# Kernel tuning notes

Hardware: AMD Instinct MI355X
Metric: run time of the kernel (lower is better)

## Reference

```python
import jax, jax.numpy as jnp
import numpy as np

T = 128          # target_size
START = 126      # tag_map['start_token']
STOP = 127       # tag_map['stop_token'] == 'end_token'
NEG = -10000.0


def setup_inputs() -> dict:
    key = jax.random.key(0)
    k1, k2, k3 = jax.random.split(key, 3)
    B, S = 256, 512
    feats = jax.random.normal(k1, (B, S, T), dtype=jnp.float32)
    transitions = jax.random.normal(k2, (T, T), dtype=jnp.float32)
    # constraints from __init__: nothing transitions into start, nothing leaves end
    transitions = transitions.at[START, :].set(NEG)
    transitions = transitions.at[:, STOP].set(NEG)
    targets = jax.random.randint(k3, (B, S), 0, 126, dtype=jnp.int32)
    return {"feats": feats, "transitions": transitions, "targets": targets}


def _crf_nll(feats, transitions, targets):
    B, S, _ = feats.shape
    # ---- forward algorithm (log partition) ----
    init = jnp.full((B, T), NEG, dtype=feats.dtype).at[:, START].set(0.0)

    def step(fv, f_t):  # fv [B,T], f_t [B,T]
        # new[b, tag] = logsumexp_prev(fv[b, prev] + trans[tag, prev]) + f_t[b, tag]
        new = jax.nn.logsumexp(fv[:, None, :] + transitions[None, :, :], axis=2) + f_t
        return new, None

    fv, _ = jax.lax.scan(step, init, jnp.swapaxes(feats, 0, 1))  # scan over S
    alpha = jax.nn.logsumexp(fv + transitions[STOP][None, :], axis=1)  # [B]

    # ---- gold path score ----
    start_col = jnp.full((B, 1), START, dtype=targets.dtype)
    tags_ext = jnp.concatenate([start_col, targets], axis=1)  # [B, S+1]
    trans_score = transitions[tags_ext[:, 1:], tags_ext[:, :-1]].sum(axis=1)  # [B]
    emit_score = jnp.take_along_axis(feats, targets[..., None].astype(jnp.int32), axis=2)[..., 0].sum(axis=1)
    gold = trans_score + emit_score + transitions[STOP, tags_ext[:, -1]]  # [B]

    # module returns gold_score - alpha
    return gold - alpha


def reference(feats, transitions, targets):
    return _crf_nll(feats, transitions, targets)
```

## Files before the change

### kernel.cpp

```cpp
#include <hip/hip_runtime.h>
#include <math.h>

#define TT 128
#define SS 512
#define NB 256
#define START_TAG 126
#define STOP_TAG 127
#define NEGV -10000.0f

__device__ __forceinline__ float rlane(float v, int lane) {
    return __int_as_float(__builtin_amdgcn_readlane(__float_as_int(v), lane));
}
__device__ __forceinline__ float wave_max(float v) {
#pragma unroll
    for (int off = 32; off >= 1; off >>= 1) v = fmaxf(v, __shfl_xor(v, off));
    return v;
}
__device__ __forceinline__ float wave_sum(float v) {
#pragma unroll
    for (int off = 32; off >= 1; off >>= 1) v += __shfl_xor(v, off);
    return v;
}

__global__ __launch_bounds__(512, 2) void crf_fwd_kernel(
    const float* __restrict__ feats,
    const float* __restrict__ trans,
    const int*   __restrict__ targets,
    float*       __restrict__ out)
{
    const int t = threadIdx.x;
    const int b = blockIdx.x;
    const int w = t >> 6;
    const int l = t & 63;
    const int group = w >> 2;
    const int g = w & 3;
    const int base = (g & 1) << 5;
    const float gsel = group ? 0.f : 1.f;
    const float gnot = group ? 1.f : 0.f;

    __shared__ float2 part[2][8][64];
    __shared__ float redz[8];
    __shared__ float galpha;

    float2 E2[32];
    if (group == 0) {
        const float* r0 = trans + l * TT + (g << 5);
        const float* r1 = trans + (l + 64) * TT + (g << 5);
#pragma unroll
        for (int k = 0; k < 32; k += 4) {
            float4 a0 = *reinterpret_cast<const float4*>(r0 + k);
            float4 a1 = *reinterpret_cast<const float4*>(r1 + k);
            E2[k + 0] = make_float2(__expf(a0.x), __expf(a1.x));
            E2[k + 1] = make_float2(__expf(a0.y), __expf(a1.y));
            E2[k + 2] = make_float2(__expf(a0.z), __expf(a1.z));
            E2[k + 3] = make_float2(__expf(a0.w), __expf(a1.w));
        }
    } else {
        const float* rc = trans + (g << 5) * TT + l;
#pragma unroll
        for (int k = 0; k < 32; ++k) {
            E2[k] = make_float2(__expf(rc[k * TT]), __expf(rc[k * TT + 64]));
        }
    }

    const size_t bst = (size_t)b * (SS * TT);
    const float* fb = feats + bst + l;

#define FIDX(i) (group ? (510 - (i)) : (i))
    float fx0 = fb[(size_t)FIDX(0) * TT], fy0 = fb[(size_t)FIDX(0) * TT + 64];
    float fx1 = fb[(size_t)FIDX(1) * TT], fy1 = fb[(size_t)FIDX(1) * TT + 64];
    float fx2 = fb[(size_t)FIDX(2) * TT], fy2 = fb[(size_t)FIDX(2) * TT + 64];
    float fx3 = fb[(size_t)FIDX(3) * TT], fy3 = fb[(size_t)FIDX(3) * TT + 64];
    const int ii = group ? 511 : 0;
    float fInx = fb[(size_t)ii * TT], fIny = fb[(size_t)ii * TT + 64];
#undef FIDX

    float statex, statey;
    if (group == 0) {
        statex = NEGV;
        statey = (l == 62) ? 0.f : NEGV;
    } else {
        statex = trans[STOP_TAG * TT + l];
        statey = trans[STOP_TAG * TT + l + 64];
    }
    float argx = fmaf(fInx, gnot, statex);
    float argy = fmaf(fIny, gnot, statey);
    float M = group ? rlane(argx, 0) : 0.f;
    float psel = __expf(((g < 2) ? argx : argy) - M);

#define STEP(P)                                                           \
    {                                                                     \
        int sn = group ? (506 - s - (P)) : (s + 4 + (P));                 \
        float fnx = fb[(size_t)sn * TT];                                  \
        float fny = fb[(size_t)sn * TT + 64];                             \
        float ax = 0.f, ay = 0.f;                                         \
        _Pragma("unroll")                                                 \
        for (int k = 0; k < 32; ++k) {                                    \
            float pk = rlane(psel, base + k);                             \
            ax = fmaf(pk, E2[k].x, ax);                                   \
            ay = fmaf(pk, E2[k].y, ay);                                   \
        }                                                                 \
        part[P][w][l] = make_float2(ax, ay);                              \
        __syncthreads();                                                  \
        float2 c1 = part[P][w ^ 1][l];                                    \
        float2 c2 = part[P][w ^ 2][l];                                    \
        float2 c3 = part[P][w ^ 3][l];                                    \
        float tx = (ax + c1.x) + (c2.x + c3.x);                           \
        float ty = (ay + c1.y) + (c2.y + c3.y);                           \
        statex = fmaf(fx0, gsel, __logf(tx) + M);                         \
        statey = fmaf(fy0, gsel, __logf(ty) + M);                         \
        float agx = fmaf(fx0, gnot, statex);                              \
        float agy = fmaf(fy0, gnot, statey);                              \
        M = rlane(agx, 0);                                                \
        psel = __expf(((g < 2) ? agx : agy) - M);                         \
        fx0 = fx1; fy0 = fy1; fx1 = fx2; fy1 = fy2;                       \
        fx2 = fx3; fy2 = fy3; fx3 = fnx; fy3 = fny;                       \
    }

    for (int s = 0; s < SS / 2; s += 2) {
        STEP(0)
        STEP(1)
    }
#undef STEP

    __syncthreads();
    if (w == 4) part[0][0][l] = make_float2(statex, statey);

    {
        const int* tg = targets + b * SS;
        int cur  = tg[t];
        int prev = (t == 0) ? START_TAG : tg[t - 1];
        float gs = trans[cur * TT + prev] + feats[bst + (size_t)t * TT + cur];
        if (t == 0) gs += trans[STOP_TAG * TT + tg[SS - 1]];
        gs = wave_sum(gs);
        if (l == 0) redz[w] = gs;
    }
    __syncthreads();

    if (w == 0) {
        float2 bb = part[0][0][l];
        float vx = statex + bb.x;
        float vy = statey + bb.y;
        float m = wave_max(fmaxf(vx, vy));
        float e = __expf(vx - m) + __expf(vy - m);
        e = wave_sum(e);
        if (l == 0) galpha = m + __logf(e);
    }
    __syncthreads();

    if (t == 0) {
        float gold = ((redz[0] + redz[1]) + (redz[2] + redz[3]))
                   + ((redz[4] + redz[5]) + (redz[6] + redz[7]));
        out[b] = gold - galpha;
    }
}

extern "C" void kernel_launch(void* const* d_in, const int* in_sizes, int n_in,
                              void* d_out, int out_size, void* d_ws, size_t ws_size,
                              hipStream_t stream) {
    const float* feats   = (const float*)d_in[0];
    const float* trans   = (const float*)d_in[1];
    const int*   targets = (const int*)d_in[2];
    float*       out     = (float*)d_out;
    crf_fwd_kernel<<<dim3(NB), dim3(512), 0, stream>>>(feats, trans, targets, out);
}
```

Before: 264.1 us.

## Use base-2 log domain, LDS broadcast of probabilities, and packed FMA in CRF forward

Switches the forward recursion to base-2 log space by pre-scaling emissions and transitions by log2(e), so the raw exp2/log hardware instructions are used without extra multiplies. It replaces the 32 per-step readlane broadcasts with each wave writing its exp values to shared memory and reading them back as float4. The inner product uses packed two-wide FMAs over four independent accumulators, which shortens the dependency chain. The wave still reads its own shared-memory slice with no barrier between the write and the read. Base-2 math also adds small rounding differences.

```diff
diff --git a/kernel.cpp b/kernel.cpp
--- a/kernel.cpp
+++ b/kernel.cpp
@@ -1,5 +1,4 @@
 #include <hip/hip_runtime.h>
-#include <math.h>
 
 #define TT 128
 #define SS 512
@@ -7,6 +6,14 @@
 #define START_TAG 126
 #define STOP_TAG 127
 #define NEGV -10000.0f
+#define LOG2E 1.4426950408889634f
+#define LN2   0.6931471805599453f
+
+typedef float v2 __attribute__((ext_vector_type(2)));
+
+__device__ __forceinline__ float ex2(float x) { return __builtin_amdgcn_exp2f(x); }
+__device__ __forceinline__ float lg2(float x) { return __builtin_amdgcn_logf(x); }
+__device__ __forceinline__ float exn(float x) { return __builtin_amdgcn_exp2f(x * LOG2E); }
 
 __device__ __forceinline__ float rlane(float v, int lane) {
     return __int_as_float(__builtin_amdgcn_readlane(__float_as_int(v), lane));
@@ -34,15 +41,15 @@
     const int l = t & 63;
     const int group = w >> 2;
     const int g = w & 3;
-    const int base = (g & 1) << 5;
     const float gsel = group ? 0.f : 1.f;
     const float gnot = group ? 1.f : 0.f;
 
-    __shared__ float2 part[2][8][64];
+    __shared__ __align__(16) float pbuf[8][128];
+    __shared__ v2 part[2][8][64];
     __shared__ float redz[8];
     __shared__ float galpha;
 
-    float2 E2[32];
+    v2 E2[32];
     if (group == 0) {
         const float* r0 = trans + l * TT + (g << 5);
         const float* r1 = trans + (l + 64) * TT + (g << 5);
@@ -50,29 +57,31 @@
         for (int k = 0; k < 32; k += 4) {
             float4 a0 = *reinterpret_cast<const float4*>(r0 + k);
             float4 a1 = *reinterpret_cast<const float4*>(r1 + k);
-            E2[k + 0] = make_float2(__expf(a0.x), __expf(a1.x));
-            E2[k + 1] = make_float2(__expf(a0.y), __expf(a1.y));
-            E2[k + 2] = make_float2(__expf(a0.z), __expf(a1.z));
-            E2[k + 3] = make_float2(__expf(a0.w), __expf(a1.w));
+            E2[k + 0] = (v2){exn(a0.x), exn(a1.x)};
+            E2[k + 1] = (v2){exn(a0.y), exn(a1.y)};
+            E2[k + 2] = (v2){exn(a0.z), exn(a1.z)};
+            E2[k + 3] = (v2){exn(a0.w), exn(a1.w)};
         }
     } else {
         const float* rc = trans + (g << 5) * TT + l;
 #pragma unroll
         for (int k = 0; k < 32; ++k) {
-            E2[k] = make_float2(__expf(rc[k * TT]), __expf(rc[k * TT + 64]));
+            E2[k] = (v2){exn(rc[k * TT]), exn(rc[k * TT + 64])};
         }
     }
 
     const size_t bst = (size_t)b * (SS * TT);
     const float* fb = feats + bst + l;
+    float* pwr = &pbuf[w][l];
+    const float4* pq4 = reinterpret_cast<const float4*>(&pbuf[w][g << 5]);
 
 #define FIDX(i) (group ? (510 - (i)) : (i))
-    float fx0 = fb[(size_t)FIDX(0) * TT], fy0 = fb[(size_t)FIDX(0) * TT + 64];
-    float fx1 = fb[(size_t)FIDX(1) * TT], fy1 = fb[(size_t)FIDX(1) * TT + 64];
-    float fx2 = fb[(size_t)FIDX(2) * TT], fy2 = fb[(size_t)FIDX(2) * TT + 64];
-    float fx3 = fb[(size_t)FIDX(3) * TT], fy3 = fb[(size_t)FIDX(3) * TT + 64];
+    float fx0 = fb[(size_t)FIDX(0) * TT] * LOG2E, fy0 = fb[(size_t)FIDX(0) * TT + 64] * LOG2E;
+    float fx1 = fb[(size_t)FIDX(1) * TT] * LOG2E, fy1 = fb[(size_t)FIDX(1) * TT + 64] * LOG2E;
+    float fx2 = fb[(size_t)FIDX(2) * TT] * LOG2E, fy2 = fb[(size_t)FIDX(2) * TT + 64] * LOG2E;
+    float fx3 = fb[(size_t)FIDX(3) * TT] * LOG2E, fy3 = fb[(size_t)FIDX(3) * TT + 64] * LOG2E;
     const int ii = group ? 511 : 0;
-    float fInx = fb[(size_t)ii * TT], fIny = fb[(size_t)ii * TT + 64];
+    float fInx = fb[(size_t)ii * TT] * LOG2E, fIny = fb[(size_t)ii * TT + 64] * LOG2E;
 #undef FIDX
 
     float statex, statey;
@@ -80,41 +89,45 @@
         statex = NEGV;
         statey = (l == 62) ? 0.f : NEGV;
     } else {
-        statex = trans[STOP_TAG * TT + l];
-        statey = trans[STOP_TAG * TT + l + 64];
+        statex = trans[STOP_TAG * TT + l] * LOG2E;
+        statey = trans[STOP_TAG * TT + l + 64] * LOG2E;
     }
     float argx = fmaf(fInx, gnot, statex);
     float argy = fmaf(fIny, gnot, statey);
     float M = group ? rlane(argx, 0) : 0.f;
-    float psel = __expf(((g < 2) ? argx : argy) - M);
+    pwr[0]  = ex2(argx - M);
+    pwr[64] = ex2(argy - M);
 
-#define STEP(P)                                                           \
-    {                                                                     \
-        int sn = group ? (506 - s - (P)) : (s + 4 + (P));                 \
-        float fnx = fb[(size_t)sn * TT];                                  \
-        float fny = fb[(size_t)sn * TT + 64];                             \
-        float ax = 0.f, ay = 0.f;                                         \
-        _Pragma("unroll")                                                 \
-        for (int k = 0; k < 32; ++k) {                                    \
-            float pk = rlane(psel, base + k);                             \
-            ax = fmaf(pk, E2[k].x, ax);                                   \
-            ay = fmaf(pk, E2[k].y, ay);                                   \
-        }                                                                 \
-        part[P][w][l] = make_float2(ax, ay);                              \
-        __syncthreads();                                                  \
-        float2 c1 = part[P][w ^ 1][l];                                    \
-        float2 c2 = part[P][w ^ 2][l];                                    \
-        float2 c3 = part[P][w ^ 3][l];                                    \
-        float tx = (ax + c1.x) + (c2.x + c3.x);                           \
-        float ty = (ay + c1.y) + (c2.y + c3.y);                           \
-        statex = fmaf(fx0, gsel, __logf(tx) + M);                         \
-        statey = fmaf(fy0, gsel, __logf(ty) + M);                         \
-        float agx = fmaf(fx0, gnot, statex);                              \
-        float agy = fmaf(fy0, gnot, statey);                              \
-        M = rlane(agx, 0);                                                \
-        psel = __expf(((g < 2) ? agx : agy) - M);                         \
-        fx0 = fx1; fy0 = fy1; fx1 = fx2; fy1 = fy2;                       \
-        fx2 = fx3; fy2 = fy3; fx3 = fnx; fy3 = fny;                       \
+#define STEP(P)                                                             \
+    {                                                                       \
+        int sn = group ? (506 - s - (P)) : (s + 4 + (P));                   \
+        float fnx = fb[(size_t)sn * TT] * LOG2E;                            \
+        float fny = fb[(size_t)sn * TT + 64] * LOG2E;                       \
+        v2 a0 = (v2){0.f, 0.f}, a1 = a0, a2 = a0, a3 = a0;                  \
+        _Pragma("unroll")                                                   \
+        for (int j = 0; j < 8; ++j) {                                       \
+            float4 q = pq4[j];                                              \
+            a0 = __builtin_elementwise_fma((v2){q.x, q.x}, E2[4*j+0], a0);  \
+            a1 = __builtin_elementwise_fma((v2){q.y, q.y}, E2[4*j+1], a1);  \
+            a2 = __builtin_elementwise_fma((v2){q.z, q.z}, E2[4*j+2], a2);  \
+            a3 = __builtin_elementwise_fma((v2){q.w, q.w}, E2[4*j+3], a3);  \
+        }                                                                   \
+        v2 acc = (a0 + a1) + (a2 + a3);                                     \
+        part[P][w][l] = acc;                                                \
+        __syncthreads();                                                    \
+        v2 c1 = part[P][w ^ 1][l];                                          \
+        v2 c2 = part[P][w ^ 2][l];                                          \
+        v2 c3 = part[P][w ^ 3][l];                                          \
+        v2 tot = (acc + c1) + (c2 + c3);                                    \
+        statex = fmaf(fx0, gsel, lg2(tot.x) + M);                           \
+        statey = fmaf(fy0, gsel, lg2(tot.y) + M);                           \
+        float agx = fmaf(fx0, gnot, statex);                                \
+        float agy = fmaf(fy0, gnot, statey);                                \
+        M = rlane(agx, 0);                                                  \
+        pwr[0]  = ex2(agx - M);                                             \
+        pwr[64] = ex2(agy - M);                                             \
+        fx0 = fx1; fy0 = fy1; fx1 = fx2; fy1 = fy2;                         \
+        fx2 = fx3; fy2 = fy3; fx3 = fnx; fy3 = fny;                         \
     }
 
     for (int s = 0; s < SS / 2; s += 2) {
@@ -124,7 +137,7 @@
 #undef STEP
 
     __syncthreads();
-    if (w == 4) part[0][0][l] = make_float2(statex, statey);
+    if (w == 4) part[0][0][l] = (v2){statex, statey};
 
     {
         const int* tg = targets + b * SS;
@@ -138,13 +151,13 @@
     __syncthreads();
 
     if (w == 0) {
-        float2 bb = part[0][0][l];
+        v2 bb = part[0][0][l];
         float vx = statex + bb.x;
         float vy = statey + bb.y;
         float m = wave_max(fmaxf(vx, vy));
-        float e = __expf(vx - m) + __expf(vy - m);
+        float e = ex2(vx - m) + ex2(vy - m);
         e = wave_sum(e);
-        if (l == 0) galpha = m + __logf(e);
+        if (l == 0) galpha = (m + lg2(e)) * LN2;
     }
     __syncthreads();
 
```

New measurement: 234.7 us. 11.1% less time.
